# Kernel tuning notes

Measured on AMD Instinct MI355X. Metric: run time of the kernel, lower is better.

## Reference

```python
import jax, jax.numpy as jnp
import numpy as np

SCALES = (1.0, 0.5, 0.25, 0.125)
POOLED_H, POOLED_W = 14, 14


def _convert_boxes(b):
    # bbox cols [0,1,3,4,6] -> (cx, cy, w, h, ry); lidar coords mapped to the
    # 200x176 BEV grid exactly as in convert_to_roi_list_format.
    cx = b[:, 0] * 175.0 / 70.4 + 0.5
    cy = (b[:, 1] + 40.0) * 199.0 / 80.0 + 0.5
    w = b[:, 3] * 175.0 / 70.4
    h = b[:, 4] * 199.0 / 80.0
    ang = b[:, 6]
    ids = jnp.zeros_like(cx)  # batch id hardcoded to 0, as in the torch code
    return jnp.stack([ids, cx, cy, w, h, ang], axis=1)  # [N,6]


def _bilinear(feat, y, x):
    # feat: [C,H,W]; y, x: [N,PH,PW] sample coordinates. ROIAlign semantics:
    # samples more than one pixel outside the map contribute zero; otherwise
    # clamp to the border and bilinearly interpolate.
    C, H, W = feat.shape
    valid = (y > -1.0) & (y < H) & (x > -1.0) & (x < W)
    y = jnp.clip(y, 0.0, H - 1)
    x = jnp.clip(x, 0.0, W - 1)
    y0 = jnp.floor(y).astype(jnp.int32)
    x0 = jnp.floor(x).astype(jnp.int32)
    y1 = jnp.minimum(y0 + 1, H - 1)
    x1 = jnp.minimum(x0 + 1, W - 1)
    ly = y - y0
    lx = x - x0
    hy = 1.0 - ly
    hx = 1.0 - lx
    v = (feat[:, y0, x0] * (hy * hx) + feat[:, y0, x1] * (hy * lx)
         + feat[:, y1, x0] * (ly * hx) + feat[:, y1, x1] * (ly * lx))  # [C,N,PH,PW]
    return jnp.where(valid, v, jnp.zeros_like(v))


def _rroi_align(feat, rois, scale):
    # feat: [C,H,W]; rois: [N,6] = (id, cx, cy, w, h, theta). One bilinear
    # sample at the center of each rotated output bin (RROIAlign affine map).
    cx = rois[:, 1] * scale
    cy = rois[:, 2] * scale
    rw = rois[:, 3] * scale
    rh = rois[:, 4] * scale
    th = rois[:, 5]
    # bin-center offsets in the box's local frame, in [-0.5, 0.5)
    fw = (jnp.arange(POOLED_W, dtype=feat.dtype) + 0.5) / POOLED_W - 0.5
    fh = (jnp.arange(POOLED_H, dtype=feat.dtype) + 0.5) / POOLED_H - 0.5
    lx = fw[None, None, :] * rw[:, None, None]  # [N,1,PW]
    ly = fh[None, :, None] * rh[:, None, None]  # [N,PH,1]
    c = jnp.cos(th)[:, None, None]
    s = jnp.sin(th)[:, None, None]
    x = cx[:, None, None] + lx * c - ly * s  # [N,PH,PW]
    y = cy[:, None, None] + lx * s + ly * c
    return jnp.transpose(_bilinear(feat, y, x), (1, 0, 2, 3))  # [N,C,PH,PW]


def setup_inputs() -> dict:
    key = jax.random.key(0)
    ks = jax.random.split(key, 8)
    d = {}
    shapes = [(1, 256, 200, 176), (1, 256, 100, 88), (1, 256, 50, 44), (1, 256, 25, 22)]
    for i, sh in enumerate(shapes):
        d[f"x{i}"] = jax.random.normal(ks[i], sh, dtype=jnp.float32)
    for i in range(4):
        u = jax.random.uniform(ks[4 + i], (512, 7), dtype=jnp.float32)
        bx = u[:, 0] * 60.0 + 5.0        # lidar x in [5, 65] m
        by = u[:, 1] * 70.0 - 35.0       # lidar y in [-35, 35] m
        bz = u[:, 2]
        bw = u[:, 3] * 2.0 + 1.5         # width ~ [1.5, 3.5] m
        bl = u[:, 4] * 4.0 + 3.0         # length ~ [3, 7] m
        bh = u[:, 5]
        ry = u[:, 6] * (2.0 * np.pi) - np.pi
        d[f"b{i}"] = jnp.stack([bx, by, bz, bw, bl, bh, ry], axis=1)
    return d


def reference(x0, x1, x2, x3, b0, b1, b2, b3):
    feats = (x0, x1, x2, x3)
    boxes = (b0, b1, b2, b3)
    outs = [_rroi_align(f[0], _convert_boxes(b), sc)
            for f, b, sc in zip(feats, boxes, SCALES)]
    return jnp.concatenate(outs, axis=0)  # [4*N, C, PH, PW]
```

## Files before the change

kernel.cpp:

```cpp
#include <hip/hip_runtime.h>

#define POOLED 14
#define NPOS   196
#define NCH    256
#define NQUAD  49

typedef float f2a __attribute__((ext_vector_type(2), aligned(4)));
typedef float f4  __attribute__((ext_vector_type(4)));

__global__ __launch_bounds__(256)
void rroi_align_kernel(const float* __restrict__ f0, const float* __restrict__ f1,
                       const float* __restrict__ f2, const float* __restrict__ f3,
                       const float* __restrict__ b0, const float* __restrict__ b1,
                       const float* __restrict__ b2, const float* __restrict__ b3,
                       float* __restrict__ out)
{
    __shared__ f4   s_w[NPOS];
    __shared__ int2 s_o[NPOS];

    const int blk = blockIdx.x;
    const int level = blk >> 9;
    const int roi = blk & 511;
    const int tid = threadIdx.x;

    const float* feat; const float* box; int H; int W; float scale;
    switch (level) {
      case 0:  feat = f0; box = b0; H = 200; W = 176; scale = 1.0f;    break;
      case 1:  feat = f1; box = b1; H = 100; W = 88;  scale = 0.5f;    break;
      case 2:  feat = f2; box = b2; H = 50;  W = 44;  scale = 0.25f;   break;
      default: feat = f3; box = b3; H = 25;  W = 22;  scale = 0.125f;  break;
    }

    if (tid < NPOS) {
        const float* bp = box + roi * 7;
        const float bx = bp[0], by = bp[1], bw = bp[3], bl = bp[4], ry = bp[6];

        const float cx = (bx * 175.0f / 70.4f + 0.5f) * scale;
        const float cy = ((by + 40.0f) * 199.0f / 80.0f + 0.5f) * scale;
        const float rw = (bw * 175.0f / 70.4f) * scale;
        const float rh = (bl * 199.0f / 80.0f) * scale;
        const float cth = cosf(ry), sth = sinf(ry);

        const int ph = tid / POOLED;
        const int pw = tid - ph * POOLED;
        const float fw = ((float)pw + 0.5f) / (float)POOLED - 0.5f;
        const float fh = ((float)ph + 0.5f) / (float)POOLED - 0.5f;
        const float lx = fw * rw;
        const float ly = fh * rh;
        const float x = cx + lx * cth - ly * sth;
        const float y = cy + lx * sth + ly * cth;

        const bool valid = (y > -1.0f) & (y < (float)H) & (x > -1.0f) & (x < (float)W);
        const float yc = fminf(fmaxf(y, 0.0f), (float)(H - 1));
        const float xc = fminf(fmaxf(x, 0.0f), (float)(W - 1));
        const int y0 = (int)floorf(yc);
        const int x0 = (int)floorf(xc);
        const int y1 = min(y0 + 1, H - 1);
        const float dy = yc - (float)y0;
        const float dx = xc - (float)x0;
        const float hy = 1.0f - dy, hx = 1.0f - dx;

        float w00 = hy * hx, w01 = hy * dx, w10 = dy * hx, w11 = dy * dx;
        if (!valid) { w00 = 0.0f; w01 = 0.0f; w10 = 0.0f; w11 = 0.0f; }

        const int xb = min(x0, W - 2);
        if (x0 == W - 1) {
            float t;
            t = w00; w00 = w01; w01 = t;
            t = w10; w10 = w11; w11 = t;
        }

        const int slot = (tid & 3) * NQUAD + (tid >> 2);
        s_w[slot] = (f4){w00, w01, w10, w11};
        s_o[slot] = make_int2(y0 * W + xb, y1 * W + xb);
    }
    __syncthreads();

    const int HW  = H * W;
    const int HW5 = 5 * HW, HW6 = 6 * HW;

    int c = tid / NQUAD;
    int q = tid - c * NQUAD;
    const float* __restrict__ fc = feat + c * HW;
    float* po = out + (size_t)blk * (NCH * NPOS) + tid * 4;

    #pragma unroll 1
    for (int it = 0; it < NQUAD; ++it) {
        f4 r;
        {
            const f4 w = s_w[q];                 const int2 o = s_o[q];
            const f2a a = *(const f2a*)(fc + o.x);
            const f2a b = *(const f2a*)(fc + o.y);
            r.x = a.x * w.x + a.y * w.y + b.x * w.z + b.y * w.w;
        }
        {
            const f4 w = s_w[NQUAD + q];         const int2 o = s_o[NQUAD + q];
            const f2a a = *(const f2a*)(fc + o.x);
            const f2a b = *(const f2a*)(fc + o.y);
            r.y = a.x * w.x + a.y * w.y + b.x * w.z + b.y * w.w;
        }
        {
            const f4 w = s_w[2 * NQUAD + q];     const int2 o = s_o[2 * NQUAD + q];
            const f2a a = *(const f2a*)(fc + o.x);
            const f2a b = *(const f2a*)(fc + o.y);
            r.z = a.x * w.x + a.y * w.y + b.x * w.z + b.y * w.w;
        }
        {
            const f4 w = s_w[3 * NQUAD + q];     const int2 o = s_o[3 * NQUAD + q];
            const f2a a = *(const f2a*)(fc + o.x);
            const f2a b = *(const f2a*)(fc + o.y);
            r.w = a.x * w.x + a.y * w.y + b.x * w.z + b.y * w.w;
        }
        __builtin_nontemporal_store(r, (f4*)po);

        q += 11;
        int step = HW5;
        if (q >= NQUAD) { q -= NQUAD; step = HW6; }
        fc += step;
        po += 1024;
    }
}

extern "C" void kernel_launch(void* const* d_in, const int* in_sizes, int n_in,
                              void* d_out, int out_size, void* d_ws, size_t ws_size,
                              hipStream_t stream)
{
    const float* f0 = (const float*)d_in[0];
    const float* f1 = (const float*)d_in[1];
    const float* f2 = (const float*)d_in[2];
    const float* f3 = (const float*)d_in[3];
    const float* b0 = (const float*)d_in[4];
    const float* b1 = (const float*)d_in[5];
    const float* b2 = (const float*)d_in[6];
    const float* b3 = (const float*)d_in[7];
    float* out = (float*)d_out;

    rroi_align_kernel<<<2048, 256, 0, stream>>>(f0, f1, f2, f3, b0, b1, b2, b3, out);
}
```

Before: 549.5 us.

## Stage ROI bounding-box feature patch in LDS and interpolate from shared memory

Each block computes the axis-aligned bounding box of its rotated ROI and cooperatively copies that feature patch for a group of channels into shared memory. Bilinear samples are then read from LDS instead of scattered global gathers, with swizzled per-sample metadata and packed offsets. The goal is to turn irregular global loads into coalesced patch loads plus reuse. The cost is extra passes, syncthreads and patch-load overhead. It also relies on the patch fitting in 9216 floats and on 16-bit offsets, which can fail for large boxes.

```diff
diff --git a/kernel.cpp b/kernel.cpp
--- a/kernel.cpp
+++ b/kernel.cpp
@@ -2,11 +2,13 @@
 
 #define POOLED 14
 #define NPOS   196
-#define NCH    256
 #define NQUAD  49
+#define SF_CAP 9216
+#define META_N 200
 
-typedef float f2a __attribute__((ext_vector_type(2), aligned(4)));
-typedef float f4  __attribute__((ext_vector_type(4)));
+typedef float f4 __attribute__((ext_vector_type(4)));
+
+__device__ __forceinline__ int swz(int s) { return s ^ ((s >> 3) & 7); }
 
 __global__ __launch_bounds__(256)
 void rroi_align_kernel(const float* __restrict__ f0, const float* __restrict__ f1,
@@ -15,8 +17,8 @@
                        const float* __restrict__ b2, const float* __restrict__ b3,
                        float* __restrict__ out)
 {
-    __shared__ f4   s_w[NPOS];
-    __shared__ int2 s_o[NPOS];
+    __shared__ float s_f[SF_CAP];
+    __shared__ f4    s_meta[META_N];
 
     const int blk = blockIdx.x;
     const int level = blk >> 9;
@@ -30,23 +32,37 @@
       case 2:  feat = f2; box = b2; H = 50;  W = 44;  scale = 0.25f;   break;
       default: feat = f3; box = b3; H = 25;  W = 22;  scale = 0.125f;  break;
     }
+    const int G     = 16 << level;
+    const int NPASS = 16 >> level;
+    const int HW    = H * W;
+
+    const float* bp = box + roi * 7;
+    const float cx  = (bp[0] * 175.0f / 70.4f + 0.5f) * scale;
+    const float cy  = ((bp[1] + 40.0f) * 199.0f / 80.0f + 0.5f) * scale;
+    const float rw  = (bp[3] * 175.0f / 70.4f) * scale;
+    const float rh  = (bp[4] * 199.0f / 80.0f) * scale;
+    const float cth = cosf(bp[6]), sth = sinf(bp[6]);
+
+    const float ex = 0.5f * (fabsf(rw * cth) + fabsf(rh * sth));
+    const float ey = 0.5f * (fabsf(rw * sth) + fabsf(rh * cth));
+    const int Xlo = min(max((int)floorf(cx - ex), 0), W - 2);
+    const int Xhi = min(W - 1, max((int)floorf(cx + ex) + 1, Xlo + 1));
+    const int Ylo = min(max((int)floorf(cy - ey), 0), H - 1);
+    const int Yhi = min(H - 1, max((int)floorf(cy + ey) + 1, Ylo + 1));
+    const int bw = Xhi - Xlo + 1;
+    const int bh = Yhi - Ylo + 1;
+    const int SP = bw * bh;
+
+    const unsigned M1 = (unsigned)(4294967296.0 / (double)SP) + 1u;
+    const unsigned M2 = 262144u / (unsigned)bw + 1u;
 
     if (tid < NPOS) {
-        const float* bp = box + roi * 7;
-        const float bx = bp[0], by = bp[1], bw = bp[3], bl = bp[4], ry = bp[6];
-
-        const float cx = (bx * 175.0f / 70.4f + 0.5f) * scale;
-        const float cy = ((by + 40.0f) * 199.0f / 80.0f + 0.5f) * scale;
-        const float rw = (bw * 175.0f / 70.4f) * scale;
-        const float rh = (bl * 199.0f / 80.0f) * scale;
-        const float cth = cosf(ry), sth = sinf(ry);
-
         const int ph = tid / POOLED;
         const int pw = tid - ph * POOLED;
-        const float fw = ((float)pw + 0.5f) / (float)POOLED - 0.5f;
-        const float fh = ((float)ph + 0.5f) / (float)POOLED - 0.5f;
-        const float lx = fw * rw;
-        const float ly = fh * rh;
+        const float fwx = ((float)pw + 0.5f) / (float)POOLED - 0.5f;
+        const float fhy = ((float)ph + 0.5f) / (float)POOLED - 0.5f;
+        const float lx = fwx * rw;
+        const float ly = fhy * rh;
         const float x = cx + lx * cth - ly * sth;
         const float y = cy + lx * sth + ly * cth;
 
@@ -56,68 +72,64 @@
         const int y0 = (int)floorf(yc);
         const int x0 = (int)floorf(xc);
         const int y1 = min(y0 + 1, H - 1);
-        const float dy = yc - (float)y0;
-        const float dx = xc - (float)x0;
-        const float hy = 1.0f - dy, hx = 1.0f - dx;
+        const float dyw = yc - (float)y0;
+        float dxw = xc - (float)x0;
 
-        float w00 = hy * hx, w01 = hy * dx, w10 = dy * hx, w11 = dy * dx;
-        if (!valid) { w00 = 0.0f; w01 = 0.0f; w10 = 0.0f; w11 = 0.0f; }
+        const float m = valid ? 1.0f : 0.0f;
+        const float A = (1.0f - dyw) * m;
+        const float B = dyw * m;
 
-        const int xb = min(x0, W - 2);
-        if (x0 == W - 1) {
-            float t;
-            t = w00; w00 = w01; w01 = t;
-            t = w10; w10 = w11; w11 = t;
+        int xb = x0;
+        if (x0 == W - 1) { xb = W - 2; dxw = 1.0f; }
+
+        const unsigned o0 = (unsigned)((y0 - Ylo) * bw + (xb - Xlo));
+        const unsigned o1 = (unsigned)((y1 - Ylo) * bw + (xb - Xlo));
+        const int slot = (tid & 3) * NQUAD + (tid >> 2);
+        s_meta[swz(slot)] = (f4){dxw, A, B, __uint_as_float(o0 | (o1 << 16))};
+    }
+
+    float* const out_roi = out + (size_t)blk * (256 * NPOS);
+    const int GITER = (G * NQUAD + 255) >> 8;
+
+    for (int pass = 0; pass < NPASS; ++pass) {
+        const int cbase = pass * G;
+        const float* __restrict__ fpass = feat + (size_t)cbase * HW;
+
+        const int E = G * SP;
+        for (int el = tid; el < E; el += 256) {
+            const int g   = (int)__umulhi((unsigned)el, M1);
+            const int rem = el - g * SP;
+            const int ry  = (int)(((unsigned)rem * M2) >> 18);
+            const int rx  = rem - ry * bw;
+            s_f[el] = fpass[g * HW + (Ylo + ry) * W + (Xlo + rx)];
         }
+        __syncthreads();
 
-        const int slot = (tid & 3) * NQUAD + (tid >> 2);
-        s_w[slot] = (f4){w00, w01, w10, w11};
-        s_o[slot] = make_int2(y0 * W + xb, y1 * W + xb);
-    }
-    __syncthreads();
-
-    const int HW  = H * W;
-    const int HW5 = 5 * HW, HW6 = 6 * HW;
-
-    int c = tid / NQUAD;
-    int q = tid - c * NQUAD;
-    const float* __restrict__ fc = feat + c * HW;
-    float* po = out + (size_t)blk * (NCH * NPOS) + tid * 4;
-
-    #pragma unroll 1
-    for (int it = 0; it < NQUAD; ++it) {
-        f4 r;
-        {
-            const f4 w = s_w[q];                 const int2 o = s_o[q];
-            const f2a a = *(const f2a*)(fc + o.x);
-            const f2a b = *(const f2a*)(fc + o.y);
-            r.x = a.x * w.x + a.y * w.y + b.x * w.z + b.y * w.w;
+        const int TMAX = G * NQUAD;
+        #pragma unroll 1
+        for (int it = 0; it < GITER; ++it) {
+            const int t = it * 256 + tid;
+            if (t < TMAX) {
+                const int c = t / NQUAD;
+                const int q = t - c * NQUAD;
+                const float* __restrict__ fb = s_f + c * SP;
+                f4 r;
+                #pragma unroll
+                for (int j = 0; j < 4; ++j) {
+                    const f4 md = s_meta[swz(j * NQUAD + q)];
+                    const float dxw = md.x, A = md.y, B = md.z;
+                    const unsigned pk = __float_as_uint(md.w);
+                    const int o0 = (int)(pk & 0xffffu);
+                    const int o1 = (int)(pk >> 16);
+                    const float hx = 1.0f - dxw;
+                    const float t0 = fb[o0], t1 = fb[o0 + 1];
+                    const float u0 = fb[o1], u1 = fb[o1 + 1];
+                    r[j] = A * (t0 * hx + t1 * dxw) + B * (u0 * hx + u1 * dxw);
+                }
+                __builtin_nontemporal_store(r, (f4*)(out_roi + (size_t)4 * (cbase * NQUAD + t)));
+            }
         }
-        {
-            const f4 w = s_w[NQUAD + q];         const int2 o = s_o[NQUAD + q];
-            const f2a a = *(const f2a*)(fc + o.x);
-            const f2a b = *(const f2a*)(fc + o.y);
-            r.y = a.x * w.x + a.y * w.y + b.x * w.z + b.y * w.w;
-        }
-        {
-            const f4 w = s_w[2 * NQUAD + q];     const int2 o = s_o[2 * NQUAD + q];
-            const f2a a = *(const f2a*)(fc + o.x);
-            const f2a b = *(const f2a*)(fc + o.y);
-            r.z = a.x * w.x + a.y * w.y + b.x * w.z + b.y * w.w;
-        }
-        {
-            const f4 w = s_w[3 * NQUAD + q];     const int2 o = s_o[3 * NQUAD + q];
-            const f2a a = *(const f2a*)(fc + o.x);
-            const f2a b = *(const f2a*)(fc + o.y);
-            r.w = a.x * w.x + a.y * w.y + b.x * w.z + b.y * w.w;
-        }
-        __builtin_nontemporal_store(r, (f4*)po);
-
-        q += 11;
-        int step = HW5;
-        if (q >= NQUAD) { q -= NQUAD; step = HW6; }
-        fc += step;
-        po += 1024;
+        __syncthreads();
     }
 }
 
```

New measurement: 540.0 us. No clear change (-1.7%).
